# Performance work log

Measured on AMD Instinct MI355X. Metric: run time of the kernel, lower is better.

## Reference

```python
import jax, jax.numpy as jnp
import numpy as np
from jax import lax

T_STEPS = 16
TAU = 2.0
ALPHA = 4.0  # sigmoid surrogate sharpness
BN_EPS = 1e-5


def conv1d(x, w, b, stride, pad):
    # x: [N,C,L], w: [O,I,K]
    y = lax.conv_general_dilated(x, w, (stride,), [(pad, pad)],
                                 dimension_numbers=('NCH', 'OIH', 'NCH'))
    return y + b[None, :, None]


def maxpool1d(x):  # kernel 3, stride 2, pad 1 (pad value -inf via init)
    return lax.reduce_window(x, -jnp.inf, lax.max, (1, 1, 3), (1, 1, 2),
                             [(0, 0), (0, 0), (1, 1)])


def spike(x):  # heaviside forward (surrogate only matters for bwd)
    return (x >= 0).astype(x.dtype)


def lif(x_seq):
    # multi-step LIF: v += (x - v)/tau (v_reset=0), spike at v>=1, hard reset, detach_reset
    def step(v, x):
        v = v + (x - v) / TAU
        s = spike(v - 1.0)
        v = v * (1.0 - lax.stop_gradient(s))
        return v, s
    _, s_seq = lax.scan(step, jnp.zeros_like(x_seq[0]), x_seq)
    return s_seq


def seq_apply(f, xs):
    # apply stateless layer over [T,B,...] by folding T into batch
    T, B = xs.shape[0], xs.shape[1]
    y = f(xs.reshape((T * B,) + xs.shape[2:]))
    return y.reshape((T, B) + y.shape[1:])


def setup_inputs() -> dict:
    key = jax.random.key(0)
    ks = jax.random.split(key, 12)
    B, L = 256, 4097
    inp = {
        'x': jax.random.normal(ks[0], (B, L), jnp.float32),
        'conv0_w': jax.random.normal(ks[1], (16, 1, 7), jnp.float32) * 0.2,
        'conv0_b': jax.random.normal(ks[2], (16,), jnp.float32) * 0.1,
        'bn_g': jnp.ones((16,), jnp.float32),
        'bn_b': jnp.zeros((16,), jnp.float32),
        'bn_m': jax.random.normal(ks[3], (16,), jnp.float32) * 0.1,
        'bn_v': jnp.ones((16,), jnp.float32),
        'conv1_w': jax.random.normal(ks[4], (32, 16, 5), jnp.float32) * 0.1,
        'conv1_b': jax.random.normal(ks[5], (32,), jnp.float32) * 0.1,
        'conv2_w': jax.random.normal(ks[6], (64, 32, 3), jnp.float32) * 0.1,
        'conv2_b': jax.random.normal(ks[7], (64,), jnp.float32) * 0.1,
        'fc1_w': jax.random.normal(ks[8], (32, 64), jnp.float32) * 0.12,
        'fc1_b': jax.random.normal(ks[9], (32,), jnp.float32) * 0.1,
        'fc2_w': jax.random.normal(ks[10], (5, 32), jnp.float32) * 0.17,
        'fc2_b': jax.random.normal(ks[11], (5,), jnp.float32) * 0.1,
    }
    return inp


def reference(x, conv0_w, conv0_b, bn_g, bn_b, bn_m, bn_v,
              conv1_w, conv1_b, conv2_w, conv2_b,
              fc1_w, fc1_b, fc2_w, fc2_b):
    # ---- static encoder ----
    h = x[:, None, :]                                  # [B,1,4097]
    h = conv1d(h, conv0_w, conv0_b, 2, 3)              # [B,16,2049]
    h = (h - bn_m[None, :, None]) * lax.rsqrt(bn_v + BN_EPS)[None, :, None] \
        * bn_g[None, :, None] + bn_b[None, :, None]
    h = jax.nn.relu(h)
    h = maxpool1d(h)                                   # [B,16,1025]
    # ---- repeat over T timesteps ----
    hs = jnp.broadcast_to(h[None], (T_STEPS,) + h.shape)  # [T,B,16,1025]
    # ---- spiking trunk ----
    hs = seq_apply(lambda a: conv1d(a, conv1_w, conv1_b, 2, 2), hs)  # [T,B,32,513]
    hs = lif(hs)
    hs = seq_apply(maxpool1d, hs)                      # [T,B,32,257]
    hs = seq_apply(lambda a: conv1d(a, conv2_w, conv2_b, 2, 1), hs)  # [T,B,64,129]
    hs = lif(hs)
    # dropout: identity (inference); adaptive avg pool to 1 + flatten
    hs = hs.mean(axis=-1)                              # [T,B,64]
    # ---- classifier ----
    hs = jnp.einsum('tbd,od->tbo', hs, fc1_w) + fc1_b  # [T,B,32]
    hs = lif(hs)
    hs = jnp.einsum('tbd,od->tbo', hs, fc2_w) + fc2_b  # [T,B,5]
    return hs.mean(axis=0)                             # [B,5]
```

## Files before the change

### kernel.cpp

```cpp
#include <hip/hip_runtime.h>
#include <math.h>


#define NB 256
#define LX 4097
#define LQ 2049
#define LP 1025
#define LJ1 513
#define LP1 257
#define LJ2 129

#define M1S 520
#define S2R 132
#define HSW 260

typedef float f32x4 __attribute__((ext_vector_type(4)));

__global__ __launch_bounds__(256) void kF_front(const float* __restrict__ x,
                                                const float* __restrict__ w0,
                                                const float* __restrict__ b0,
                                                const float* __restrict__ bng,
                                                const float* __restrict__ bnb,
                                                const float* __restrict__ bnm,
                                                const float* __restrict__ bnv,
                                                const float* __restrict__ w1,
                                                const float* __restrict__ b1,
                                                unsigned short* __restrict__ m1,
                                                const float* __restrict__ w2,
                                                float* __restrict__ w2t2) {
  __shared__ __align__(16) float xs[1052];
  __shared__ __align__(16) float hs[8 * HSW];
  __shared__ __align__(16) float wl[2560];
  __shared__ float w0s[112];
  __shared__ float cpar[64];
  __shared__ float rs_l[16];
  int bid = blockIdx.x;
  int b = bid / 5, jt = bid % 5;
  int J0 = jt * 128;
  int Pstart = 2 * J0 - 2;
  int tid = threadIdx.x;

  if (tid < 16) rs_l[tid] = (float)(1.0 / sqrt((double)bnv[tid] + 1e-5));
  {
    const float* xb = x + (size_t)b * LX;
    int xoff = 4 * Pstart - 5;
    for (int i = tid; i < 1052; i += 256) {
      int gi = xoff + i;
      xs[i] = (gi >= 0 && gi < LX) ? xb[gi] : 0.f;
    }
    for (int i = tid; i < 2560; i += 256) {
      int c = i & 31, r = i >> 5;
      wl[i] = w1[c * 80 + r];
    }
    if (tid < 112) w0s[tid] = w0[tid];
    if (tid >= 128 && tid < 192) {
      int i = tid - 128;
      int c = i >> 2, e = i & 3;
      float v = (e == 0) ? bnm[c] : (e == 1) ? bng[c] : (e == 2) ? bnb[c] : b0[c];
      cpar[i] = v;
    }
  }
  __syncthreads();

  int c = tid & 31, jg = tid >> 5;
  int jbase = J0 + jg * 16;
  bool active = (jbase <= 512);
  float acc[16];
#pragma unroll
  for (int i = 0; i < 16; ++i) acc[i] = 0.f;

  for (int half = 0; half < 2; ++half) {
    {
      int c2l = tid >> 5;
      int g2 = tid & 31;
      int cc = half * 8 + c2l;
      float m = cpar[4 * cc], g = cpar[4 * cc + 1], bb = cpar[4 * cc + 2],
            bc = cpar[4 * cc + 3];
      float rs = rs_l[cc];
      float wv[7];
#pragma unroll
      for (int k = 0; k < 7; ++k) wv[k] = w0s[cc * 7 + k];
#pragma unroll
      for (int i = 0; i < 9; ++i) {
        int dp = g2 * 9 + i;
        if (dp < 261) {
          int p = Pstart + dp;
          float hm = 0.f;
          if (p >= 0 && p < LP) {
            const f32x4* xv = (const f32x4*)(xs + 4 * dp);
            f32x4 a = xv[0], bq = xv[1], cq = xv[2];
            float win[12] = {a.x, a.y, a.z, a.w, bq.x, bq.y, bq.z, bq.w,
                             cq.x, cq.y, cq.z, cq.w};
            float best = -INFINITY;
#pragma unroll
            for (int dq = -1; dq <= 1; ++dq) {
              int q = 2 * p + dq;
              if (q < 0 || q >= LQ) continue;
              float s = 0.f;
              int base = 2 * dq + 2;
#pragma unroll
              for (int k = 0; k < 7; ++k) s = fmaf(win[base + k], wv[k], s);
              float y = s + bc;
              y = (y - m) * rs * g + bb;
              y = fmaxf(y, 0.f);
              best = fmaxf(best, y);
            }
            hm = best;
          }
          hs[c2l * HSW + dp] = hm;
        }
      }
    }
    __syncthreads();

    if (active) {
      for (int icl = 0; icl < 8; ++icl) {
        int ic = half * 8 + icl;
        float win[36];
        const f32x4* row = (const f32x4*)(hs + icl * HSW + 32 * jg);
#pragma unroll
        for (int i = 0; i < 9; ++i) {
          f32x4 v = row[i];
          win[4 * i] = v.x; win[4 * i + 1] = v.y;
          win[4 * i + 2] = v.z; win[4 * i + 3] = v.w;
        }
        float wv[5];
#pragma unroll
        for (int k = 0; k < 5; ++k) wv[k] = wl[(ic * 5 + k) * 32 + c];
#pragma unroll
        for (int j = 0; j < 16; ++j) {
#pragma unroll
          for (int k = 0; k < 5; ++k) acc[j] = fmaf(win[2 * j + k], wv[k], acc[j]);
        }
      }
    }
    __syncthreads();
  }

  if (active) {
    float bc = b1[c];
    unsigned mskv[16];
#pragma unroll
    for (int j = 0; j < 16; ++j) {
      float xin = acc[j] + bc;
      float v = 0.f; unsigned mm = 0;
#pragma unroll
      for (int t = 0; t < 16; ++t) {
        v = v + (xin - v) * 0.5f;
        if (v >= 1.f) { mm |= (1u << t); v = 0.f; }
      }
      mskv[j] = mm;
    }
    size_t rowo = ((size_t)b * 32 + c) * M1S + jbase;
    if (jbase + 15 < LJ1) {
      uint4 u0, u1;
      u0.x = mskv[0] | (mskv[1] << 16);
      u0.y = mskv[2] | (mskv[3] << 16);
      u0.z = mskv[4] | (mskv[5] << 16);
      u0.w = mskv[6] | (mskv[7] << 16);
      u1.x = mskv[8] | (mskv[9] << 16);
      u1.y = mskv[10] | (mskv[11] << 16);
      u1.z = mskv[12] | (mskv[13] << 16);
      u1.w = mskv[14] | (mskv[15] << 16);
      *(uint4*)(m1 + rowo) = u0;
      *(uint4*)(m1 + rowo + 8) = u1;
    } else {
      for (int j = 0; j < 16; ++j)
        if (jbase + j < LJ1) m1[rowo + j] = (unsigned short)mskv[j];
    }
  }

  if (bid < 16) {
    for (int idx = bid * 256 + tid; idx < 64 * 32 * 3; idx += 4096) {
      int k = idx % 3; int r = idx / 3; int cc = r % 32; int oc = r / 32;
      w2t2[((size_t)cc * 64 + oc) * 4 + k] = w2[idx];
    }
  }
}

__global__ __launch_bounds__(256) void kD_conv2_lif(const unsigned short* __restrict__ m1,
                                                    const float* __restrict__ w2t2,
                                                    const float* __restrict__ b2,
                                                    unsigned short* __restrict__ s2) {
  __shared__ __align__(16) float F[288 * 20];
  __shared__ unsigned mval[288];
  __shared__ unsigned short mbuf[32 * 20];
  int bid = blockIdx.x;
  int b = bid / 33, jt = bid % 33;
  int j0 = jt * 4;
  int tid = threadIdx.x;
  int w = tid >> 6;
  int lane = tid & 63;

  const unsigned short* m1b = m1 + (size_t)b * 32 * M1S;
  int qbase = 4 * j0 - 3;
  for (int i = tid; i < 1024; i += 256) {
    int c = i >> 5, u = i & 31;
    if (u < 20) {
      int q = qbase + u;
      mbuf[c * 20 + u] = (q >= 0 && q <= 512) ? m1b[(size_t)c * M1S + q] : (unsigned short)0;
    }
  }
  __syncthreads();

  for (int it = tid; it < 288; it += 256) {
    int c = it / 9, idx = it - c * 9;
    int p = 2 * j0 - 1 + idx;
    unsigned m = 0;
    if (p >= 0 && p < LP1) {
      const unsigned short* mr = mbuf + c * 20;
      int l0 = 2 * idx;
      m = (unsigned)mr[l0] | (unsigned)mr[l0 + 1] | (unsigned)mr[l0 + 2];
    }
    mval[it] = m;
    f32x4* Fr = (f32x4*)(F + it * 20);
    f32x4 f0, f1, f2, f3;
    f0.x = (float)(m & 1u);         f0.y = (float)((m >> 1) & 1u);
    f0.z = (float)((m >> 2) & 1u);  f0.w = (float)((m >> 3) & 1u);
    f1.x = (float)((m >> 4) & 1u);  f1.y = (float)((m >> 5) & 1u);
    f1.z = (float)((m >> 6) & 1u);  f1.w = (float)((m >> 7) & 1u);
    f2.x = (float)((m >> 8) & 1u);  f2.y = (float)((m >> 9) & 1u);
    f2.z = (float)((m >> 10) & 1u); f2.w = (float)((m >> 11) & 1u);
    f3.x = (float)((m >> 12) & 1u); f3.y = (float)((m >> 13) & 1u);
    f3.z = (float)((m >> 14) & 1u); f3.w = (float)((m >> 15) & 1u);
    Fr[0] = f0; Fr[1] = f1; Fr[2] = f2; Fr[3] = f3;
  }
  __syncthreads();

  unsigned bits;
  {
    bool nz = false;
    if (lane < 32) {
      int base9 = lane * 9 + 2 * w;
      nz = (mval[base9] | mval[base9 + 1] | mval[base9 + 2]) != 0u;
    }
    bits = (unsigned)__ballot(nz);
  }

  float acc[16];
#pragma unroll
  for (int t = 0; t < 16; ++t) acc[t] = 0.f;

  const f32x4* wbase = (const f32x4*)w2t2 + lane;
  while (bits) {
    int c = __builtin_ctz(bits);
    bits &= bits - 1;
    int base9 = c * 9 + 2 * w;
    unsigned mv0 = mval[base9];
    unsigned mv1 = mval[base9 + 1];
    unsigned mv2 = mval[base9 + 2];
    f32x4 wq = wbase[c * 64];
    const float* Fb = F + base9 * 20;
    if (mv0) {
      const f32x4* Fp = (const f32x4*)Fb;
      f32x4 fv[4];
      fv[0] = Fp[0]; fv[1] = Fp[1]; fv[2] = Fp[2]; fv[3] = Fp[3];
#pragma unroll
      for (int t = 0; t < 16; ++t) acc[t] = fmaf(wq.x, fv[t >> 2][t & 3], acc[t]);
    }
    if (mv1) {
      const f32x4* Fp = (const f32x4*)(Fb + 20);
      f32x4 fv[4];
      fv[0] = Fp[0]; fv[1] = Fp[1]; fv[2] = Fp[2]; fv[3] = Fp[3];
#pragma unroll
      for (int t = 0; t < 16; ++t) acc[t] = fmaf(wq.y, fv[t >> 2][t & 3], acc[t]);
    }
    if (mv2) {
      const f32x4* Fp = (const f32x4*)(Fb + 40);
      f32x4 fv[4];
      fv[0] = Fp[0]; fv[1] = Fp[1]; fv[2] = Fp[2]; fv[3] = Fp[3];
#pragma unroll
      for (int t = 0; t < 16; ++t) acc[t] = fmaf(wq.z, fv[t >> 2][t & 3], acc[t]);
    }
  }

  int j = j0 + w;
  if (j < LJ2) {
    float bc = b2[lane];
    float v = 0.f; unsigned mm = 0;
#pragma unroll
    for (int t = 0; t < 16; ++t) {
      float xin = acc[t] + bc;
      v = v + (xin - v) * 0.5f;
      if (v >= 1.f) { mm |= (1u << t); v = 0.f; }
    }
    s2[((size_t)b * S2R + j) * 64 + lane] = (unsigned short)mm;
  }
}

__global__ __launch_bounds__(256) void kE_head(const unsigned short* __restrict__ s2,
                                               const float* __restrict__ fc1w,
                                               const float* __restrict__ fc1b,
                                               const float* __restrict__ fc2w,
                                               const float* __restrict__ fc2b,
                                               float* __restrict__ out) {
  __shared__ unsigned cntL[4][16][64];
  __shared__ float meanL[16][64];
  __shared__ unsigned s3m[32];
  int b = blockIdx.x;
  int tid = threadIdx.x;
  int w = tid >> 6, lane = tid & 63;

  int j0 = (w == 0) ? 0 : 33 + 32 * (w - 1);
  int jc = (w == 0) ? 33 : 32;
  const unsigned short* base = s2 + (size_t)b * S2R * 64 + lane;
  unsigned cnt[16];
#pragma unroll
  for (int t = 0; t < 16; ++t) cnt[t] = 0;
  for (int u = 0; u < jc; ++u) {
    unsigned m = base[(size_t)(j0 + u) * 64];
#pragma unroll
    for (int t = 0; t < 16; ++t) cnt[t] += (m >> t) & 1u;
  }
#pragma unroll
  for (int t = 0; t < 16; ++t) cntL[w][t][lane] = cnt[t];
  __syncthreads();

#pragma unroll
  for (int i = 0; i < 4; ++i) {
    int idx = tid + 256 * i;
    int t = idx >> 6, oc = idx & 63;
    unsigned s = cntL[0][t][oc] + cntL[1][t][oc] + cntL[2][t][oc] + cntL[3][t][oc];
    meanL[t][oc] = (float)s / 129.f;
  }
  __syncthreads();

  if (tid < 32) {
    int o = tid;
    const float* wrow = fc1w + o * 64;
    float bb = fc1b[o];
    float v = 0.f;
    unsigned msk = 0;
    for (int t = 0; t < 16; ++t) {
      float s = 0.f;
      for (int d = 0; d < 64; ++d) s = fmaf(meanL[t][d], wrow[d], s);
      float xin = s + bb;
      v = v + (xin - v) * 0.5f;
      if (v >= 1.f) { msk |= (1u << t); v = 0.f; }
    }
    s3m[o] = msk;
  }
  __syncthreads();

  if (tid < 5) {
    int q = tid;
    const float* wrow = fc2w + q * 32;
    float bb = fc2b[q];
    float accs = 0.f;
    for (int t = 0; t < 16; ++t) {
      float s = 0.f;
      for (int o = 0; o < 32; ++o) s += (((s3m[o] >> t) & 1u) ? wrow[o] : 0.f);
      accs += (s + bb);
    }
    out[b * 5 + q] = accs / 16.f;
  }
}

extern "C" void kernel_launch(void* const* d_in, const int* in_sizes, int n_in,
                              void* d_out, int out_size, void* d_ws, size_t ws_size,
                              hipStream_t stream) {
  const float* x   = (const float*)d_in[0];
  const float* w0  = (const float*)d_in[1];
  const float* b0  = (const float*)d_in[2];
  const float* bng = (const float*)d_in[3];
  const float* bnb = (const float*)d_in[4];
  const float* bnm = (const float*)d_in[5];
  const float* bnv = (const float*)d_in[6];
  const float* w1  = (const float*)d_in[7];
  const float* b1  = (const float*)d_in[8];
  const float* w2  = (const float*)d_in[9];
  const float* b2  = (const float*)d_in[10];
  const float* f1w = (const float*)d_in[11];
  const float* f1b = (const float*)d_in[12];
  const float* f2w = (const float*)d_in[13];
  const float* f2b = (const float*)d_in[14];
  float* out = (float*)d_out;

  char* ws = (char*)d_ws;
  size_t sz_m1 = (size_t)NB * 32 * M1S * 2;
  size_t sz_s2 = (size_t)NB * S2R * 64 * 2;
  size_t off_s2 = sz_m1;
  size_t off_w2 = off_s2 + sz_s2;
  if (ws_size < off_w2 + 32768) return;

  unsigned short* m1 = (unsigned short*)ws;
  unsigned short* s2 = (unsigned short*)(ws + off_s2);
  float* w2t2 = (float*)(ws + off_w2);

  kF_front<<<NB * 5, 256, 0, stream>>>(x, w0, b0, bng, bnb, bnm, bnv, w1, b1, m1, w2, w2t2);
  kD_conv2_lif<<<NB * 33, 256, 0, stream>>>(m1, w2t2, b2, s2);
  kE_head<<<NB, 256, 0, stream>>>(s2, f1w, f1b, f2w, f2b, out);
}
```

Baseline: 116.5 us.

## Compute all 16 front-end channels in one pass with sliding-window register reuse

The front kernel now builds the pooled conv0/BN/ReLU tile for all 16 channels at once, using a doubled shared buffer, instead of two halves of 8 channels. That removes two block barriers and the half loop. Each thread now covers 17 consecutive pooled positions and slides a three-vector register window, so it loads one new float4 from LDS per position instead of three. In exchange, shared memory per block grows, which may cut occupancy, and the xs buffer is padded so the window read-ahead stays in bounds.

```diff
diff --git a/kernel.cpp b/kernel.cpp
--- a/kernel.cpp
+++ b/kernel.cpp
@@ -28,8 +28,8 @@
                                                 unsigned short* __restrict__ m1,
                                                 const float* __restrict__ w2,
                                                 float* __restrict__ w2t2) {
-  __shared__ __align__(16) float xs[1052];
-  __shared__ __align__(16) float hs[8 * HSW];
+  __shared__ __align__(16) float xs[1056];
+  __shared__ __align__(16) float hs[16 * HSW];
   __shared__ __align__(16) float wl[2560];
   __shared__ float w0s[112];
   __shared__ float cpar[64];
@@ -44,7 +44,7 @@
   {
     const float* xb = x + (size_t)b * LX;
     int xoff = 4 * Pstart - 5;
-    for (int i = tid; i < 1052; i += 256) {
+    for (int i = tid; i < 1056; i += 256) {
       int gi = xoff + i;
       xs[i] = (gi >= 0 && gi < LX) ? xb[gi] : 0.f;
     }
@@ -62,62 +62,59 @@
   }
   __syncthreads();
 
-  int c = tid & 31, jg = tid >> 5;
-  int jbase = J0 + jg * 16;
-  bool active = (jbase <= 512);
-  float acc[16];
-#pragma unroll
-  for (int i = 0; i < 16; ++i) acc[i] = 0.f;
-
-  for (int half = 0; half < 2; ++half) {
-    {
-      int c2l = tid >> 5;
-      int g2 = tid & 31;
-      int cc = half * 8 + c2l;
-      float m = cpar[4 * cc], g = cpar[4 * cc + 1], bb = cpar[4 * cc + 2],
-            bc = cpar[4 * cc + 3];
-      float rs = rs_l[cc];
-      float wv[7];
-#pragma unroll
-      for (int k = 0; k < 7; ++k) wv[k] = w0s[cc * 7 + k];
-#pragma unroll
-      for (int i = 0; i < 9; ++i) {
-        int dp = g2 * 9 + i;
-        if (dp < 261) {
-          int p = Pstart + dp;
-          float hm = 0.f;
-          if (p >= 0 && p < LP) {
-            const f32x4* xv = (const f32x4*)(xs + 4 * dp);
-            f32x4 a = xv[0], bq = xv[1], cq = xv[2];
-            float win[12] = {a.x, a.y, a.z, a.w, bq.x, bq.y, bq.z, bq.w,
-                             cq.x, cq.y, cq.z, cq.w};
-            float best = -INFINITY;
-#pragma unroll
-            for (int dq = -1; dq <= 1; ++dq) {
-              int q = 2 * p + dq;
-              if (q < 0 || q >= LQ) continue;
-              float s = 0.f;
-              int base = 2 * dq + 2;
-#pragma unroll
-              for (int k = 0; k < 7; ++k) s = fmaf(win[base + k], wv[k], s);
-              float y = s + bc;
-              y = (y - m) * rs * g + bb;
-              y = fmaxf(y, 0.f);
-              best = fmaxf(best, y);
-            }
-            hm = best;
-          }
-          hs[c2l * HSW + dp] = hm;
+  {
+    int c2 = tid >> 4, g2 = tid & 15;
+    float m = cpar[4 * c2], g = cpar[4 * c2 + 1], bb = cpar[4 * c2 + 2],
+          bc = cpar[4 * c2 + 3];
+    float rs = rs_l[c2];
+    float wv[7];
+#pragma unroll
+    for (int k = 0; k < 7; ++k) wv[k] = w0s[c2 * 7 + k];
+    int dp0 = g2 * 17;
+    const f32x4* xv = (const f32x4*)xs;
+    f32x4 q0 = xv[dp0], q1 = xv[dp0 + 1], q2 = xv[dp0 + 2];
+#pragma unroll
+    for (int i = 0; i < 17; ++i) {
+      int dp = dp0 + i;
+      if (dp >= 261) break;
+      int p = Pstart + dp;
+      float hm = 0.f;
+      if (p >= 0 && p < LP) {
+        float win[12] = {q0.x, q0.y, q0.z, q0.w, q1.x, q1.y, q1.z, q1.w,
+                         q2.x, q2.y, q2.z, q2.w};
+        float best = -INFINITY;
+#pragma unroll
+        for (int dq = -1; dq <= 1; ++dq) {
+          int q = 2 * p + dq;
+          if (q < 0 || q >= LQ) continue;
+          float s = 0.f;
+          int base = 2 * dq + 2;
+#pragma unroll
+          for (int k = 0; k < 7; ++k) s = fmaf(win[base + k], wv[k], s);
+          float y = s + bc;
+          y = (y - m) * rs * g + bb;
+          y = fmaxf(y, 0.f);
+          best = fmaxf(best, y);
         }
+        hm = best;
       }
-    }
-    __syncthreads();
-
-    if (active) {
-      for (int icl = 0; icl < 8; ++icl) {
-        int ic = half * 8 + icl;
+      hs[c2 * HSW + dp] = hm;
+      q0 = q1; q1 = q2; q2 = xv[dp + 3];
+    }
+  }
+  __syncthreads();
+
+  {
+    int c = tid & 31, jg = tid >> 5;
+    int jbase = J0 + jg * 16;
+    if (jbase <= 512) {
+      float acc[16];
+#pragma unroll
+      for (int i = 0; i < 16; ++i) acc[i] = 0.f;
+
+      for (int ic = 0; ic < 16; ++ic) {
         float win[36];
-        const f32x4* row = (const f32x4*)(hs + icl * HSW + 32 * jg);
+        const f32x4* row = (const f32x4*)(hs + ic * HSW + 32 * jg);
 #pragma unroll
         for (int i = 0; i < 9; ++i) {
           f32x4 v = row[i];
@@ -133,40 +130,37 @@
           for (int k = 0; k < 5; ++k) acc[j] = fmaf(win[2 * j + k], wv[k], acc[j]);
         }
       }
-    }
-    __syncthreads();
-  }
-
-  if (active) {
-    float bc = b1[c];
-    unsigned mskv[16];
-#pragma unroll
-    for (int j = 0; j < 16; ++j) {
-      float xin = acc[j] + bc;
-      float v = 0.f; unsigned mm = 0;
-#pragma unroll
-      for (int t = 0; t < 16; ++t) {
-        v = v + (xin - v) * 0.5f;
-        if (v >= 1.f) { mm |= (1u << t); v = 0.f; }
+
+      float bc = b1[c];
+      unsigned mskv[16];
+#pragma unroll
+      for (int j = 0; j < 16; ++j) {
+        float xin = acc[j] + bc;
+        float v = 0.f; unsigned mm = 0;
+#pragma unroll
+        for (int t = 0; t < 16; ++t) {
+          v = v + (xin - v) * 0.5f;
+          if (v >= 1.f) { mm |= (1u << t); v = 0.f; }
+        }
+        mskv[j] = mm;
       }
-      mskv[j] = mm;
-    }
-    size_t rowo = ((size_t)b * 32 + c) * M1S + jbase;
-    if (jbase + 15 < LJ1) {
-      uint4 u0, u1;
-      u0.x = mskv[0] | (mskv[1] << 16);
-      u0.y = mskv[2] | (mskv[3] << 16);
-      u0.z = mskv[4] | (mskv[5] << 16);
-      u0.w = mskv[6] | (mskv[7] << 16);
-      u1.x = mskv[8] | (mskv[9] << 16);
-      u1.y = mskv[10] | (mskv[11] << 16);
-      u1.z = mskv[12] | (mskv[13] << 16);
-      u1.w = mskv[14] | (mskv[15] << 16);
-      *(uint4*)(m1 + rowo) = u0;
-      *(uint4*)(m1 + rowo + 8) = u1;
-    } else {
-      for (int j = 0; j < 16; ++j)
-        if (jbase + j < LJ1) m1[rowo + j] = (unsigned short)mskv[j];
+      size_t rowo = ((size_t)b * 32 + c) * M1S + jbase;
+      if (jbase + 15 < LJ1) {
+        uint4 u0, u1;
+        u0.x = mskv[0] | (mskv[1] << 16);
+        u0.y = mskv[2] | (mskv[3] << 16);
+        u0.z = mskv[4] | (mskv[5] << 16);
+        u0.w = mskv[6] | (mskv[7] << 16);
+        u1.x = mskv[8] | (mskv[9] << 16);
+        u1.y = mskv[10] | (mskv[11] << 16);
+        u1.z = mskv[12] | (mskv[13] << 16);
+        u1.w = mskv[14] | (mskv[15] << 16);
+        *(uint4*)(m1 + rowo) = u0;
+        *(uint4*)(m1 + rowo + 8) = u1;
+      } else {
+        for (int j = 0; j < 16; ++j)
+          if (jbase + j < LJ1) m1[rowo + j] = (unsigned short)mskv[j];
+      }
     }
   }
 
```

Result: faster. 112.2 us (-3.7%).
